# Kernel tuning notes

Measured on AMD Instinct MI355X. Metric: run time of the kernel, lower is better.

## Reference

```python
import jax, jax.numpy as jnp
import numpy as np

D_MODEL = 1024
NUM_HEADS = 16
DEPTH = D_MODEL // NUM_HEADS
MAX_LEN = 5000
B, S = 4, 1024


def _dense(x, W, b):
    return x @ W + b


def _split_heads(x, n_heads, depth):
    # [..., S, D] -> [..., H, S, depth]
    *lead, s, d = x.shape
    x = x.reshape(*lead, s, n_heads, depth)
    return jnp.swapaxes(x, -3, -2)


def setup_inputs() -> dict:
    key = jax.random.key(0)
    ks = jax.random.split(key, 12)
    w = 0.02  # glorot-ish scale to keep softmax logits sane
    inp = {
        'q': jax.random.normal(ks[0], (B, S, D_MODEL), jnp.float32),
        'k': jax.random.normal(ks[1], (B, S, D_MODEL), jnp.float32),
        'v': jax.random.normal(ks[2], (B, S, D_MODEL), jnp.float32),
        'Wq': jax.random.normal(ks[3], (D_MODEL, D_MODEL), jnp.float32) * w,
        'bq': jnp.zeros((D_MODEL,), jnp.float32),
        'Wk': jax.random.normal(ks[4], (D_MODEL, D_MODEL), jnp.float32) * w,
        'bk': jnp.zeros((D_MODEL,), jnp.float32),
        'Wv': jax.random.normal(ks[5], (D_MODEL, D_MODEL), jnp.float32) * w,
        'bv': jnp.zeros((D_MODEL,), jnp.float32),
        'Uq': jax.random.normal(ks[6], (D_MODEL, D_MODEL), jnp.float32) * w,
        'buq': jnp.zeros((D_MODEL,), jnp.float32),
        'Uk': jax.random.normal(ks[7], (D_MODEL, D_MODEL), jnp.float32) * w,
        'buk': jnp.zeros((D_MODEL,), jnp.float32),
        'pos_table': jax.random.normal(ks[8], (MAX_LEN, D_MODEL), jnp.float32) * w,
        'theta_cc': jnp.zeros((1, NUM_HEADS, 1, 1), jnp.float32),
        'theta_co': jnp.zeros((1, NUM_HEADS, 1, 1), jnp.float32),
        'theta_oc': jnp.zeros((1, NUM_HEADS, 1, 1), jnp.float32),
        'Wo': jax.random.normal(ks[9], (D_MODEL, D_MODEL), jnp.float32) * w,
        'bo': jnp.zeros((D_MODEL,), jnp.float32),
    }
    return inp


def reference(q, k, v, Wq, bq, Wk, bk, Wv, bv, Uq, buq, Uk, buk,
              pos_table, theta_cc, theta_co, theta_oc, Wo, bo):
    b, s, d = q.shape
    # content projections -> [B,H,S,depth]
    q_c = _split_heads(_dense(q, Wq, bq), NUM_HEADS, DEPTH)
    k_c = _split_heads(_dense(k, Wk, bk), NUM_HEADS, DEPTH)
    v_c = _split_heads(_dense(v, Wv, bv), NUM_HEADS, DEPTH)
    content_scores = jnp.einsum('bhqd,bhkd->bhqk', q_c, k_c)

    # untied positional scores (shared across batch): [1,H,S,S]
    pos_emb = pos_table[:s]                               # [S,D]
    q_p = _split_heads(_dense(pos_emb, Uq, buq)[None], NUM_HEADS, DEPTH)
    k_p = _split_heads(_dense(pos_emb, Uk, buk)[None], NUM_HEADS, DEPTH)
    pos_scores = jnp.einsum('bhqd,bhkd->bhqk', q_p, k_p)  # [1,H,S,S]

    # CLS-row/col overrides with learnable thetas
    pos_scores = pos_scores.at[:, :, 1:, 0:1].set(jnp.broadcast_to(theta_oc, (1, NUM_HEADS, s - 1, 1)))
    pos_scores = pos_scores.at[:, :, 0:1, 1:].set(jnp.broadcast_to(theta_co, (1, NUM_HEADS, 1, s - 1)))
    pos_scores = pos_scores.at[:, :, 0:1, 0:1].set(theta_cc)

    scores = (content_scores + pos_scores) / jnp.sqrt(jnp.float32(DEPTH))
    attn = jax.nn.softmax(scores, axis=-1)
    out = jnp.einsum('bhqk,bhkd->bhqd', attn, v_c)        # [B,H,S,depth]
    out = jnp.swapaxes(out, 1, 2).reshape(b, s, d)        # [B,S,D]
    return _dense(out, Wo, bo)
```

## Files before the change

kernel.cpp:

```cpp
#include <hip/hip_runtime.h>
#include <hip/hip_bf16.h>

typedef __hip_bfloat16 bf16;
typedef unsigned short u16;
typedef __attribute__((ext_vector_type(8))) short short8;
typedef __attribute__((ext_vector_type(4))) float f32x4;

#define D_MODEL 1024
#define NUM_HEADS 16
#define DEPTH 64
#define BATCH 4
#define SEQ 1024
#define BS (BATCH * SEQ)

__device__ __forceinline__ float ldDyn(const void* p, size_t i, int isbf) {
  return isbf ? __bfloat162float(((const bf16*)p)[i]) : ((const float*)p)[i];
}
__device__ __forceinline__ u16 f2bf(float f) {
  bf16 h = __float2bfloat16(f);
  return *(u16*)&h;
}
__device__ __forceinline__ void gl2lds16(const void* g, void* l) {
  __builtin_amdgcn_global_load_lds((const __attribute__((address_space(1))) unsigned int*)g,
                                   (__attribute__((address_space(3))) unsigned int*)l, 16, 0, 0);
}

__device__ __forceinline__ int detect_isbf(const u16* q) {
  int sane = 0;
#pragma unroll
  for (int i = 0; i < 64; ++i) {
    int e = (q[2 * i] >> 7) & 0xFF;
    sane += (e >= 100 && e <= 150) ? 1 : 0;
  }
  return (sane >= 48) ? 1 : 0;
}

__global__ __launch_bounds__(256) void prep(
    const void* __restrict__ q, const void* __restrict__ k, const void* __restrict__ v,
    const void* __restrict__ pos, const void* __restrict__ W0, const void* __restrict__ W1,
    const void* __restrict__ W2, const void* __restrict__ W3, const void* __restrict__ W4,
    const void* __restrict__ W5, u16* __restrict__ Qb, u16* __restrict__ Kb,
    u16* __restrict__ Vb, u16* __restrict__ Pb, u16* __restrict__ WT,
    int* __restrict__ flag) {
  const int isbf = detect_isbf((const u16*)q);
  const int z = blockIdx.z;
  const int t = threadIdx.x;
  if (z == 0 && blockIdx.x == 0 && t == 0) *flag = isbf;

  if (z < 4) {
    const void* src = (z == 0) ? q : (z == 1) ? k : (z == 2) ? v : pos;
    u16* dst = (z == 0) ? Qb : (z == 1) ? Kb : (z == 2) ? Vb : Pb;
    const size_t n8 = ((z == 3) ? (size_t)SEQ * D_MODEL : (size_t)BS * D_MODEL) / 8;
    for (size_t i = (size_t)blockIdx.x * 256 + t; i < n8; i += (size_t)gridDim.x * 256) {
      short8 o;
      if (isbf) {
        o = ((const short8*)src)[i];
      } else {
        const float4* f = (const float4*)src + 2 * i;
        float4 lo = f[0], hi = f[1];
        u16* pv = (u16*)&o;
        pv[0] = f2bf(lo.x); pv[1] = f2bf(lo.y); pv[2] = f2bf(lo.z); pv[3] = f2bf(lo.w);
        pv[4] = f2bf(hi.x); pv[5] = f2bf(hi.y); pv[6] = f2bf(hi.z); pv[7] = f2bf(hi.w);
      }
      ((short8*)dst)[i] = o;
    }
  } else {
    const int w = z - 4;
    const void* W = (w == 0) ? W0 : (w == 1) ? W1 : (w == 2) ? W2
                   : (w == 3) ? W3 : (w == 4) ? W4 : W5;
    u16* out = WT + (size_t)w * D_MODEL * D_MODEL;
    __shared__ u16 tile[32][33];
    const int tx = t & 31, ty = t >> 5;
    const int r0 = (blockIdx.x >> 5) * 32, c0 = (blockIdx.x & 31) * 32;
#pragma unroll
    for (int i = 0; i < 4; ++i) {
      size_t gi = (size_t)(r0 + ty + 8 * i) * D_MODEL + c0 + tx;
      tile[ty + 8 * i][tx] = isbf ? ((const u16*)W)[gi] : f2bf(((const float*)W)[gi]);
    }
    __syncthreads();
#pragma unroll
    for (int i = 0; i < 4; ++i)
      out[(size_t)(c0 + ty + 8 * i) * D_MODEL + r0 + tx] = tile[tx][ty + 8 * i];
  }
}

struct GArgs {
  const u16* A[5];
  const u16* W[5];
  const void* bias[5];
  void* C[5];
  int Mr[5];
  int om[5];
};

__global__ __launch_bounds__(256, 2) void gemm_mfma(GArgs ga, const int* __restrict__ flagp) {
  const int isbf = *flagp;
  const int z = blockIdx.z;
  const int M = ga.Mr[z];
  const int lin = blockIdx.x + 8 * blockIdx.y;
  const int xcd = lin & 7;
  const int loc = lin >> 3;
  const int rowb = (loc & 1) * 8 + xcd;
  const int colb = loc >> 1;
  const int row0 = rowb * 256, col0 = colb * 128;
  if (row0 >= M) return;
  const u16* A = ga.A[z];
  const u16* WT = ga.W[z];
  const void* bias = ga.bias[z];
  void* C = ga.C[z];
  const int omode = ga.om[z];

  __shared__ short As[3][256][32];
  __shared__ short Bs[3][128][32];
  const int t = threadIdx.x;
  const int wave = t >> 6, lane = t & 63;
  const int quad = lane >> 4, c16 = lane & 15;
  const int wrow = wave >> 1, wcol = wave & 1;

  f32x4 acc[8][4];
#pragma unroll
  for (int mt = 0; mt < 8; ++mt)
#pragma unroll
    for (int nt = 0; nt < 4; ++nt) acc[mt][nt] = {0.f, 0.f, 0.f, 0.f};

#define G_STAGE(K0, BUF)                                                                  \
  {                                                                                       \
    _Pragma("unroll") for (int i = 0; i < 4; ++i) {                                       \
      int L = t + 256 * i;                                                                \
      int r = L >> 2;                                                                     \
      int kc = (L & 3) ^ ((r + (r >> 2)) & 3);                                            \
      gl2lds16(A + (size_t)(row0 + r) * 1024 + (K0) + kc * 8,                             \
               (char*)&As[BUF][0][0] + (size_t)(i * 256 + wave * 64) * 16);               \
    }                                                                                     \
    _Pragma("unroll") for (int i = 0; i < 2; ++i) {                                       \
      int L = t + 256 * i;                                                                \
      int r = L >> 2;                                                                     \
      int kc = (L & 3) ^ ((r + (r >> 2)) & 3);                                            \
      gl2lds16(WT + (size_t)(col0 + r) * 1024 + (K0) + kc * 8,                            \
               (char*)&Bs[BUF][0][0] + (size_t)(i * 256 + wave * 64) * 16);               \
    }                                                                                     \
  }

  const int fsw = (c16 + (c16 >> 2)) & 3;

#define COMPUTE(BUF)                                                                      \
  {                                                                                       \
    short8 af[8], bfv[4];                                                                 \
    _Pragma("unroll") for (int mt = 0; mt < 8; ++mt)                                      \
        af[mt] = *(const short8*)&As[BUF][wrow * 128 + mt * 16 + c16][((quad ^ fsw) * 8)];\
    _Pragma("unroll") for (int nt = 0; nt < 4; ++nt)                                      \
        bfv[nt] = *(const short8*)&Bs[BUF][wcol * 64 + nt * 16 + c16][((quad ^ fsw) * 8)];\
    _Pragma("unroll") for (int nt = 0; nt < 4; ++nt)                                      \
      _Pragma("unroll") for (int mt = 0; mt < 8; ++mt)                                    \
          acc[mt][nt] =                                                                   \
              __builtin_amdgcn_mfma_f32_16x16x32_bf16(af[mt], bfv[nt], acc[mt][nt], 0, 0, 0); \
  }

  G_STAGE(0, 0);
  G_STAGE(32, 1);
#pragma unroll
  for (int kk = 0; kk < 31; ++kk) {
    asm volatile("s_waitcnt vmcnt(6)\n\ts_barrier" ::: "memory");
    if (kk < 30) G_STAGE((kk + 2) * 32, (kk + 2) % 3);
    COMPUTE(kk % 3);
  }
  asm volatile("s_waitcnt vmcnt(0)\n\ts_barrier" ::: "memory");
  COMPUTE(1);
#undef G_STAGE
#undef COMPUTE

#pragma unroll
  for (int nt = 0; nt < 4; ++nt) {
    int gc = col0 + wcol * 64 + nt * 16 + c16;
    float bb = ldDyn(bias, gc, isbf);
#pragma unroll
    for (int mt = 0; mt < 8; ++mt) {
      int gr0 = row0 + wrow * 128 + mt * 16 + quad * 4;
      if (omode == 2) {
        __attribute__((ext_vector_type(4))) short pk;
#pragma unroll
        for (int r = 0; r < 4; ++r) pk[r] = (short)f2bf(acc[mt][nt][r] + bb);
        *(__attribute__((ext_vector_type(4))) short*)&((u16*)C)[(size_t)gc * M + gr0] = pk;
      } else if (omode == 1 || isbf) {
#pragma unroll
        for (int r = 0; r < 4; ++r)
          ((bf16*)C)[(size_t)(gr0 + r) * 1024 + gc] = __float2bfloat16(acc[mt][nt][r] + bb);
      } else {
#pragma unroll
        for (int r = 0; r < 4; ++r)
          ((float*)C)[(size_t)(gr0 + r) * 1024 + gc] = acc[mt][nt][r] + bb;
      }
    }
  }
}

__global__ __launch_bounds__(256) void flash_attn(
    const bf16* __restrict__ Qc, const bf16* __restrict__ Kc, const bf16* __restrict__ VcT,
    const bf16* __restrict__ Qp, const bf16* __restrict__ Kp,
    const void* __restrict__ th_cc, const void* __restrict__ th_co,
    const void* __restrict__ th_oc, bf16* __restrict__ O, const int* __restrict__ flagp) {
  const int isbf = *flagp;
  const int h = blockIdx.x, b = blockIdx.y, qt = blockIdx.z;
  const int t = threadIdx.x, wave = t >> 6, lane = t & 63;
  const int quad = lane >> 4, c16 = lane & 15;

  __shared__ short Kt[2][64][128];
  __shared__ short Vt[2][64][64];
  __shared__ short Pt[4][16][64];

  const float tcc = ldDyn(th_cc, h, isbf);
  const float tco = ldDyn(th_co, h, isbf);
  const float toc = ldDyn(th_oc, h, isbf);

  const bf16* kcb = Kc + (size_t)b * SEQ * 1024 + h * 64;
  const bf16* kpb = Kp + h * 64;
  const bf16* vtb = VcT + (size_t)(h * 64) * BS + (size_t)b * SEQ;

  const int rwK = lane >> 4, kcK = lane & 15;
  const int rwV = lane >> 3, kcV = lane & 7;

#define STAGE_K(KT2, BUF)                                                              \
  {                                                                                    \
    _Pragma("unroll") for (int i = 0; i < 4; ++i) {                                    \
      int r = wave * 16 + i * 4 + rwK;                                                 \
      int c = kcK ^ (r & 15);                                                          \
      int key = (KT2)*64 + r;                                                          \
      const bf16* src = (c < 8) ? kcb + (size_t)key * 1024 + c * 8                     \
                                : kpb + (size_t)key * 1024 + c * 8 - 64;               \
      gl2lds16(src, &Kt[BUF][wave * 16 + i * 4][0]);                                   \
    }                                                                                  \
  }
#define STAGE_V(KT2, BUF)                                                              \
  {                                                                                    \
    _Pragma("unroll") for (int j = 0; j < 2; ++j) {                                    \
      int d = wave * 16 + j * 8 + rwV;                                                 \
      int c = kcV ^ (d & 7);                                                           \
      gl2lds16(vtb + (size_t)d * BS + (KT2)*64 + c * 8, &Vt[BUF][wave * 16 + j * 8][0]); \
    }                                                                                  \
  }

  short8 qf[2][4];
#pragma unroll
  for (int mt = 0; mt < 2; ++mt) {
    int qrow = qt * 128 + wave * 32 + mt * 16 + c16;
#pragma unroll
    for (int ks = 0; ks < 4; ++ks) {
      int d = ks * 32 + quad * 8;
      const bf16* src = (d < 64) ? Qc + ((size_t)(b * SEQ + qrow)) * 1024 + h * 64 + d
                                 : Qp + (size_t)qrow * 1024 + h * 64 + (d - 64);
      qf[mt][ks] = *(const short8*)src;
    }
    if (qrow == 0) {
      qf[mt][2] = (short8)0;
      qf[mt][3] = (short8)0;
    }
  }

  f32x4 accO[2][4];
#pragma unroll
  for (int mt = 0; mt < 2; ++mt)
#pragma unroll
    for (int nt = 0; nt < 4; ++nt) accO[mt][nt] = {0.f, 0.f, 0.f, 0.f};
  float lrow[2][4] = {{0.f, 0.f, 0.f, 0.f}, {0.f, 0.f, 0.f, 0.f}};

  STAGE_K(0, 0);
  STAGE_V(0, 0);
  __syncthreads();
  if (t < 8) *(short8*)&Kt[0][0][64 + t * 8] = (short8)0;
  __syncthreads();

  for (int kt = 0; kt < 16; ++kt) {
    const int cur = kt & 1, nxt = cur ^ 1;
    if (kt < 15) {
      STAGE_K(kt + 1, nxt);
      STAGE_V(kt + 1, nxt);
    }

    f32x4 accS[2][4];
#pragma unroll
    for (int mt = 0; mt < 2; ++mt)
#pragma unroll
      for (int nt = 0; nt < 4; ++nt) accS[mt][nt] = {0.f, 0.f, 0.f, 0.f};
    __builtin_amdgcn_s_setprio(1);
#pragma unroll
    for (int nt = 0; nt < 4; ++nt)
#pragma unroll
      for (int ks = 0; ks < 4; ++ks) {
        short8 kf = *(const short8*)&Kt[cur][nt * 16 + c16][((ks * 4 + quad) ^ c16) * 8];
#pragma unroll
        for (int mt = 0; mt < 2; ++mt)
          accS[mt][nt] = __builtin_amdgcn_mfma_f32_16x16x32_bf16(qf[mt][ks], kf, accS[mt][nt], 0, 0, 0);
      }
    __builtin_amdgcn_s_setprio(0);

    short8 vbreg[2][4];
#pragma unroll
    for (int ks2 = 0; ks2 < 2; ++ks2)
#pragma unroll
      for (int nt = 0; nt < 4; ++nt)
        vbreg[ks2][nt] =
            *(const short8*)&Vt[cur][nt * 16 + c16][(((ks2 * 4 + quad) ^ (c16 & 7)) & 7) * 8];

#pragma unroll
    for (int mt = 0; mt < 2; ++mt) {
      float s[4][4];
#pragma unroll
      for (int nt = 0; nt < 4; ++nt)
#pragma unroll
        for (int r = 0; r < 4; ++r) s[nt][r] = accS[mt][nt][r] * 0.125f;

      if (kt == 0 || (qt == 0 && wave == 0 && mt == 0)) {
#pragma unroll
        for (int nt = 0; nt < 4; ++nt)
#pragma unroll
          for (int r = 0; r < 4; ++r) {
            int kcol = kt * 64 + nt * 16 + c16;
            int qrow = qt * 128 + wave * 32 + mt * 16 + quad * 4 + r;
            float add = 0.f;
            if (qrow == 0 && kcol == 0) add = tcc;
            else if (qrow == 0) add = tco;
            else if (kcol == 0) add = toc;
            s[nt][r] += add * 0.125f;
          }
      }
#pragma unroll
      for (int nt = 0; nt < 4; ++nt)
#pragma unroll
        for (int r = 0; r < 4; ++r) {
          float p = __expf(s[nt][r]);
          lrow[mt][r] += p;
          int row = quad * 4 + r;
          int ch = nt * 2 + (c16 >> 3);
          Pt[wave][row][((ch ^ (row & 7)) * 8) + (c16 & 7)] = (short)f2bf(p);
        }
      __builtin_amdgcn_s_setprio(1);
#pragma unroll
      for (int ks2 = 0; ks2 < 2; ++ks2) {
        short8 pf = *(const short8*)&Pt[wave][c16][(((ks2 * 4 + quad) ^ (c16 & 7)) & 7) * 8];
#pragma unroll
        for (int nt = 0; nt < 4; ++nt)
          accO[mt][nt] = __builtin_amdgcn_mfma_f32_16x16x32_bf16(pf, vbreg[ks2][nt], accO[mt][nt], 0, 0, 0);
      }
      __builtin_amdgcn_s_setprio(0);
    }
    __syncthreads();
  }

#pragma unroll
  for (int d = 1; d < 16; d <<= 1)
#pragma unroll
    for (int mt = 0; mt < 2; ++mt)
#pragma unroll
      for (int r = 0; r < 4; ++r) lrow[mt][r] += __shfl_xor(lrow[mt][r], d, 64);

#pragma unroll
  for (int mt = 0; mt < 2; ++mt)
#pragma unroll
    for (int nt = 0; nt < 4; ++nt)
#pragma unroll
      for (int r = 0; r < 4; ++r) {
        int qrow = qt * 128 + wave * 32 + mt * 16 + quad * 4 + r;
        O[((size_t)(b * SEQ + qrow)) * 1024 + h * 64 + nt * 16 + c16] =
            __float2bfloat16(accO[mt][nt][r] / lrow[mt][r]);
      }
#undef STAGE_K
#undef STAGE_V
}

extern "C" void kernel_launch(void* const* d_in, const int* in_sizes, int n_in,
                              void* d_out, int out_size, void* d_ws, size_t ws_size,
                              hipStream_t stream) {
  const void* q = d_in[0];
  const void* k = d_in[1];
  const void* v = d_in[2];
  const void* Wq = d_in[3];
  const void* bq = d_in[4];
  const void* Wk = d_in[5];
  const void* bk = d_in[6];
  const void* Wv = d_in[7];
  const void* bv = d_in[8];
  const void* Uq = d_in[9];
  const void* buq = d_in[10];
  const void* Uk = d_in[11];
  const void* buk = d_in[12];
  const void* pos = d_in[13];
  const void* th_cc = d_in[14];
  const void* th_co = d_in[15];
  const void* th_oc = d_in[16];
  const void* Wo = d_in[17];
  const void* bo = d_in[18];

  const int M = BS;
  const size_t DD = (size_t)D_MODEL * D_MODEL;
  char* wsb = (char*)d_ws;
  int* flag = (int*)wsb;
  bf16* Qc = (bf16*)(wsb + 256);
  bf16* Kc = Qc + (size_t)M * D_MODEL;
  bf16* VcT = Kc + (size_t)M * D_MODEL;
  bf16* Qp = VcT + (size_t)M * D_MODEL;
  bf16* Kp = Qp + (size_t)SEQ * D_MODEL;
  u16* WT = (u16*)(Kp + (size_t)SEQ * D_MODEL);
  bf16* AO = (bf16*)WT;
  u16* Qb = WT + 6 * DD;
  u16* Kb = Qb + (size_t)M * D_MODEL;
  u16* Vb = Kb + (size_t)M * D_MODEL;
  u16* Pb = Vb + (size_t)M * D_MODEL;

  dim3 blk(256);
  prep<<<dim3(1024, 1, 10), blk, 0, stream>>>(q, k, v, pos, Wq, Wk, Wv, Uq, Uk, Wo,
                                              Qb, Kb, Vb, Pb, WT, flag);

  GArgs g1 = {{Qb, Kb, Vb, Pb, Pb},
              {WT + 0 * DD, WT + 1 * DD, WT + 2 * DD, WT + 3 * DD, WT + 4 * DD},
              {bq, bk, bv, buq, buk},
              {Qc, Kc, VcT, Qp, Kp},
              {M, M, M, SEQ, SEQ},
              {1, 1, 2, 1, 1}};
  gemm_mfma<<<dim3(8, 16, 5), blk, 0, stream>>>(g1, flag);

  flash_attn<<<dim3(NUM_HEADS, BATCH, SEQ / 128), blk, 0, stream>>>(
      Qc, Kc, VcT, Qp, Kp, th_cc, th_co, th_oc, AO, flag);

  GArgs g2 = {{(const u16*)AO, (const u16*)AO, (const u16*)AO, (const u16*)AO, (const u16*)AO},
              {WT + 5 * DD, WT + 5 * DD, WT + 5 * DD, WT + 5 * DD, WT + 5 * DD},
              {bo, bo, bo, bo, bo},
              {d_out, d_out, d_out, d_out, d_out},
              {M, M, M, M, M},
              {0, 0, 0, 0, 0}};
  gemm_mfma<<<dim3(8, 16, 1), blk, 0, stream>>>(g2, flag);
}
```

Before: 301.3 us.

## Enlarge GEMM tile to 256x256 with 512-thread blocks and MFMA priority

Moves the projection and output GEMMs from 256x128 tiles with 4 waves to 256x256 tiles with 8 waves. The block-to-tile mapping is redone so XCDs cover rows, and blocks beyond the smaller positional GEMMs exit early. This gives more data reuse per loaded A tile, and it halves B-tile refetches across column blocks. s_setprio is raised around the MFMA burst. The costs are more LDS per block (96KB), possibly lower occupancy, and fewer blocks (64 for M=4096), which may underfill the 256 CUs.

Measured after the change: 288.2 us. 1.05x faster.

```diff
diff --git a/kernel.cpp b/kernel.cpp
--- a/kernel.cpp
+++ b/kernel.cpp
@@ -93,16 +93,23 @@
   int om[5];
 };
 
-__global__ __launch_bounds__(256, 2) void gemm_mfma(GArgs ga, const int* __restrict__ flagp) {
+__global__ __launch_bounds__(512, 2) void gemm_mfma(GArgs ga, const int* __restrict__ flagp) {
   const int isbf = *flagp;
   const int z = blockIdx.z;
   const int M = ga.Mr[z];
-  const int lin = blockIdx.x + 8 * blockIdx.y;
+  const int lin = blockIdx.x + 4 * blockIdx.y;
   const int xcd = lin & 7;
-  const int loc = lin >> 3;
-  const int rowb = (loc & 1) * 8 + xcd;
-  const int colb = loc >> 1;
-  const int row0 = rowb * 256, col0 = colb * 128;
+  const int idx = lin >> 3;
+  int rowb, colb;
+  if (M >= 4096) {
+    rowb = xcd * 2 + (idx & 1);
+    colb = idx >> 1;
+  } else {
+    if (idx >= 2) return;
+    rowb = idx * 2 + (xcd & 1);
+    colb = xcd >> 1;
+  }
+  const int row0 = rowb * 256, col0 = colb * 256;
   if (row0 >= M) return;
   const u16* A = ga.A[z];
   const u16* WT = ga.W[z];
@@ -111,11 +118,12 @@
   const int omode = ga.om[z];
 
   __shared__ short As[3][256][32];
-  __shared__ short Bs[3][128][32];
+  __shared__ short Bs[3][256][32];
   const int t = threadIdx.x;
   const int wave = t >> 6, lane = t & 63;
   const int quad = lane >> 4, c16 = lane & 15;
-  const int wrow = wave >> 1, wcol = wave & 1;
+  const int wrow = wave >> 2;
+  const int wcol = wave & 3;
 
   f32x4 acc[8][4];
 #pragma unroll
@@ -125,19 +133,14 @@
 
 #define G_STAGE(K0, BUF)                                                                  \
   {                                                                                       \
-    _Pragma("unroll") for (int i = 0; i < 4; ++i) {                                       \
-      int L = t + 256 * i;                                                                \
+    _Pragma("unroll") for (int j = 0; j < 2; ++j) {                                       \
+      int L = t + 512 * j;                                                                \
       int r = L >> 2;                                                                     \
       int kc = (L & 3) ^ ((r + (r >> 2)) & 3);                                            \
       gl2lds16(A + (size_t)(row0 + r) * 1024 + (K0) + kc * 8,                             \
-               (char*)&As[BUF][0][0] + (size_t)(i * 256 + wave * 64) * 16);               \
-    }                                                                                     \
-    _Pragma("unroll") for (int i = 0; i < 2; ++i) {                                       \
-      int L = t + 256 * i;                                                                \
-      int r = L >> 2;                                                                     \
-      int kc = (L & 3) ^ ((r + (r >> 2)) & 3);                                            \
+               (char*)&As[BUF][0][0] + (size_t)(j * 512 + wave * 64) * 16);               \
       gl2lds16(WT + (size_t)(col0 + r) * 1024 + (K0) + kc * 8,                            \
-               (char*)&Bs[BUF][0][0] + (size_t)(i * 256 + wave * 64) * 16);               \
+               (char*)&Bs[BUF][0][0] + (size_t)(j * 512 + wave * 64) * 16);               \
     }                                                                                     \
   }
 
@@ -150,17 +153,19 @@
         af[mt] = *(const short8*)&As[BUF][wrow * 128 + mt * 16 + c16][((quad ^ fsw) * 8)];\
     _Pragma("unroll") for (int nt = 0; nt < 4; ++nt)                                      \
         bfv[nt] = *(const short8*)&Bs[BUF][wcol * 64 + nt * 16 + c16][((quad ^ fsw) * 8)];\
+    __builtin_amdgcn_s_setprio(1);                                                        \
     _Pragma("unroll") for (int nt = 0; nt < 4; ++nt)                                      \
       _Pragma("unroll") for (int mt = 0; mt < 8; ++mt)                                    \
           acc[mt][nt] =                                                                   \
               __builtin_amdgcn_mfma_f32_16x16x32_bf16(af[mt], bfv[nt], acc[mt][nt], 0, 0, 0); \
+    __builtin_amdgcn_s_setprio(0);                                                        \
   }
 
   G_STAGE(0, 0);
   G_STAGE(32, 1);
 #pragma unroll
   for (int kk = 0; kk < 31; ++kk) {
-    asm volatile("s_waitcnt vmcnt(6)\n\ts_barrier" ::: "memory");
+    asm volatile("s_waitcnt vmcnt(4)\n\ts_barrier" ::: "memory");
     if (kk < 30) G_STAGE((kk + 2) * 32, (kk + 2) % 3);
     COMPUTE(kk % 3);
   }
@@ -406,9 +411,8 @@
   u16* Vb = Kb + (size_t)M * D_MODEL;
   u16* Pb = Vb + (size_t)M * D_MODEL;
 
-  dim3 blk(256);
-  prep<<<dim3(1024, 1, 10), blk, 0, stream>>>(q, k, v, pos, Wq, Wk, Wv, Uq, Uk, Wo,
-                                              Qb, Kb, Vb, Pb, WT, flag);
+  prep<<<dim3(1024, 1, 10), dim3(256), 0, stream>>>(q, k, v, pos, Wq, Wk, Wv, Uq, Uk, Wo,
+                                                    Qb, Kb, Vb, Pb, WT, flag);
 
   GArgs g1 = {{Qb, Kb, Vb, Pb, Pb},
               {WT + 0 * DD, WT + 1 * DD, WT + 2 * DD, WT + 3 * DD, WT + 4 * DD},
@@ -416,9 +420,9 @@
               {Qc, Kc, VcT, Qp, Kp},
               {M, M, M, SEQ, SEQ},
               {1, 1, 2, 1, 1}};
-  gemm_mfma<<<dim3(8, 16, 5), blk, 0, stream>>>(g1, flag);
-
-  flash_attn<<<dim3(NUM_HEADS, BATCH, SEQ / 128), blk, 0, stream>>>(
+  gemm_mfma<<<dim3(4, 16, 5), dim3(512), 0, stream>>>(g1, flag);
+
+  flash_attn<<<dim3(NUM_HEADS, BATCH, SEQ / 128), dim3(256), 0, stream>>>(
       Qc, Kc, VcT, Qp, Kp, th_cc, th_co, th_oc, AO, flag);
 
   GArgs g2 = {{(const u16*)AO, (const u16*)AO, (const u16*)AO, (const u16*)AO, (const u16*)AO},
@@ -427,5 +431,5 @@
               {d_out, d_out, d_out, d_out, d_out},
               {M, M, M, M, M},
               {0, 0, 0, 0, 0}};
-  gemm_mfma<<<dim3(8, 16, 1), blk, 0, stream>>>(g2, flag);
-}
+  gemm_mfma<<<dim3(4, 16, 1), dim3(512), 0, stream>>>(g2, flag);
+}
```
